# Kernel optimization log

Hardware: AMD Instinct MI355X
Metric: run time of the kernel (lower is better)

Reference implementation:

```python
import jax, jax.numpy as jnp
import numpy as np

N_INPUT = 128
N_HIDDEN = 128

def setup_inputs() -> dict:
    key = jax.random.key(0)
    k1, k2, k3, k4, k5 = jax.random.split(key, 5)
    B, T = 64, 4096
    fan1 = N_INPUT + N_HIDDEN
    s1 = 1.0 / np.sqrt(fan1)
    s2 = 1.0 / np.sqrt(N_HIDDEN)
    return {
        "input": jax.random.normal(k1, (B, T, N_INPUT), dtype=jnp.float32),
        "W1": jax.random.uniform(k2, (N_HIDDEN, fan1), jnp.float32, -s1, s1),
        "b1": jax.random.uniform(k3, (N_HIDDEN,), jnp.float32, -s1, s1),
        "W2": jax.random.uniform(k4, (N_HIDDEN, N_HIDDEN), jnp.float32, -s2, s2),
        "b2": jax.random.uniform(k5, (N_HIDDEN,), jnp.float32, -s2, s2),
    }

def reference(input, W1, b1, W2, b2):
    # input: [B, T, n_input]; carried state h: [B, n_hidden]
    B, T, _ = input.shape
    # split linear1 weight: cat order is (h, x)
    W1h = W1[:, :N_HIDDEN]   # [H, H]
    W1x = W1[:, N_HIDDEN:]   # [H, n_input]
    # precompute input projection for all timesteps: [B, T, H]
    x_proj = jnp.einsum('bti,hi->bth', input, W1x) + b1

    def step(h, xp_t):
        h_new = jax.nn.relu(h @ W1h.T + xp_t)          # [B, H]
        out = jax.nn.relu(h_new @ W2.T + b2)            # [B, H]
        return h_new, out

    h0 = jnp.zeros((B, N_HIDDEN), dtype=input.dtype)
    _, outs = jax.lax.scan(step, h0, jnp.swapaxes(x_proj, 0, 1))  # outs: [T, B, H]
    return jnp.swapaxes(outs, 0, 1)  # [B, T, H]
```

## Files before the change

kernel.cpp:

```cpp
#include <hip/hip_runtime.h>
#include <stdint.h>

#define T_LEN 4096
#define NHID  128

typedef float    f32x4 __attribute__((ext_vector_type(4)));
typedef _Float16 f16x4 __attribute__((ext_vector_type(4)));
typedef _Float16 f16x8 __attribute__((ext_vector_type(8)));
typedef __fp16   h16x2 __attribute__((ext_vector_type(2)));
typedef uint32_t u32x2 __attribute__((ext_vector_type(2)));
typedef uint32_t u32x4 __attribute__((ext_vector_type(4)));

struct P2 { h16x2 p0, p1; };
struct P4 { h16x2 p0, p1, p2, p3; };
struct U22 { u32x2 a, b; };

static __device__ __forceinline__ f16x4 cvt_f16x4(f32x4 v) {
    P2 p;
    p.p0 = __builtin_amdgcn_cvt_pkrtz(v.x, v.y);
    p.p1 = __builtin_amdgcn_cvt_pkrtz(v.z, v.w);
    return __builtin_bit_cast(f16x4, p);
}
static __device__ __forceinline__ f16x8 cvt_f16x8(f32x4 a, f32x4 b) {
    P4 p;
    p.p0 = __builtin_amdgcn_cvt_pkrtz(a.x, a.y);
    p.p1 = __builtin_amdgcn_cvt_pkrtz(a.z, a.w);
    p.p2 = __builtin_amdgcn_cvt_pkrtz(b.x, b.y);
    p.p3 = __builtin_amdgcn_cvt_pkrtz(b.z, b.w);
    return __builtin_bit_cast(f16x8, p);
}
static __device__ __forceinline__ f32x4 relu4(f32x4 v) {
    v.x = fmaxf(v.x, 0.f); v.y = fmaxf(v.y, 0.f);
    v.z = fmaxf(v.z, 0.f); v.w = fmaxf(v.w, 0.f);
    return v;
}
static __device__ __forceinline__ u32x2 relu_pk(f32x4 v) {
    P2 p;
    p.p0 = __builtin_amdgcn_cvt_pkrtz(v.x, v.y);
    p.p1 = __builtin_amdgcn_cvt_pkrtz(v.z, v.w);
    f16x4 h = __builtin_bit_cast(f16x4, p);
    const f16x4 z = {};
    h = __builtin_elementwise_max(h, z);
    return __builtin_bit_cast(u32x2, h);
}
static __device__ __forceinline__ f32x4 unpk4(u32x2 q) {
    f16x4 h = __builtin_bit_cast(f16x4, q);
    f32x4 r = { (float)h.x, (float)h.y, (float)h.z, (float)h.w };
    return r;
}
#define MFMA32(a, b, c) __builtin_amdgcn_mfma_f32_16x16x32_f16((a), (b), (c), 0, 0, 0)
#define MFMA16(a, b, c) __builtin_amdgcn_mfma_f32_16x16x16f16((a), (b), (c), 0, 0, 0)

#define LDS_BARRIER() asm volatile("s_waitcnt lgkmcnt(0)\n\ts_barrier" ::: "memory")


__global__ __launch_bounds__(64, 2)
void xproj_kernel(const float* __restrict__ input, const float* __restrict__ W1,
                  const float* __restrict__ b1, uint32_t* __restrict__ xp) {
    const int bid = blockIdx.x;
    const int g   = bid >> 8;
    const int tc  = bid & 255;
    const int l   = threadIdx.x;
    const int c   = l & 15, u = l >> 4;

    f16x8 wa[8][4];
#pragma unroll
    for (int m = 0; m < 8; ++m) {
        const float* wr = W1 + (16 * m + c) * 256 + 128 + 8 * u;
#pragma unroll
        for (int j = 0; j < 4; ++j)
            wa[m][j] = cvt_f16x8(*(const f32x4*)(wr + 32 * j),
                                 *(const f32x4*)(wr + 32 * j + 4));
    }
    f32x4 bi[8];
#pragma unroll
    for (int m = 0; m < 8; ++m) bi[m] = *(const f32x4*)(b1 + 16 * m + 4 * u);

    const int t0 = tc * 16;
    const float* ip0 = input + (size_t)(16 * g + c) * T_LEN * NHID + 8 * u;
    uint32_t* xp0 = xp + ((size_t)g * T_LEN) * 1024 + 4 * l;
#pragma unroll 1
    for (int tt = 0; tt < 16; ++tt) {
        const int t = t0 + tt;
        const float* ip = ip0 + (size_t)t * NHID;
        f16x8 xb[4];
#pragma unroll
        for (int j = 0; j < 4; ++j)
            xb[j] = cvt_f16x8(*(const f32x4*)(ip + 32 * j),
                              *(const f32x4*)(ip + 32 * j + 4));
        u32x2 pk[8];
#pragma unroll
        for (int m = 0; m < 8; ++m) {
            f32x4 a = bi[m];
#pragma unroll
            for (int j = 0; j < 4; ++j) a = MFMA32(wa[m][j], xb[j], a);
            pk[m] = __builtin_bit_cast(u32x2, cvt_f16x4(a));
        }
        uint32_t* xpt = xp0 + (size_t)t * 1024;
#pragma unroll
        for (int q = 0; q < 4; ++q) {
            U22 qq = { pk[q], pk[q + 4] };
            *(u32x4*)(xpt + q * 256) = __builtin_bit_cast(u32x4, qq);
        }
    }
}

__global__ __launch_bounds__(320, 1)
void rec_kernel(const uint32_t* __restrict__ xp, const float* __restrict__ W1,
                uint32_t* __restrict__ hg) {
    const int g  = blockIdx.x;
    const int wv = threadIdx.x >> 6;
    const int l  = threadIdx.x & 63;
    const int c  = l & 15, u = l >> 4;

    __shared__ uint32_t hbuf[2][1024];

    for (int i = threadIdx.x; i < 1024; i += 320) hbuf[0][i] = 0;
    __syncthreads();

    if (wv < 4) {
        const int w = wv;
        f16x8 waH[2][4];
#pragma unroll
        for (int e = 0; e < 2; ++e) {
            const float* wr = W1 + (16 * (w + 4 * e) + c) * 256;
#pragma unroll
            for (int kt = 0; kt < 4; ++kt)
                waH[e][kt] = cvt_f16x8(*(const f32x4*)(wr + 16 * kt + 4 * u),
                                       *(const f32x4*)(wr + 64 + 16 * kt + 4 * u));
        }

        const uint32_t* xpl = xp + ((size_t)g * T_LEN) * 1024 + w * 256 + 4 * l;

        u32x4 xr[8];
#pragma unroll
        for (int p = 0; p < 8; ++p)
            xr[p] = *(const u32x4*)(xpl + (size_t)p * 1024);

        f16x8 own;
        {
            const u32x4 z = {0, 0, 0, 0};
            own = __builtin_bit_cast(f16x8, z);
        }

#pragma unroll 1
        for (int t8 = 0; t8 < T_LEN; t8 += 8) {
#pragma unroll
            for (int p = 0; p < 8; ++p) {
                const int t   = t8 + p;
                const int par = p & 1;
                const uint32_t* rb = &hbuf[par][0];
                u32x4 r1 = *(const u32x4*)&rb[((w + 1) & 3) * 256 + 4 * l];
                u32x4 r2 = *(const u32x4*)&rb[((w + 2) & 3) * 256 + 4 * l];
                u32x4 r3 = *(const u32x4*)&rb[((w + 3) & 3) * 256 + 4 * l];
                U22 xq = __builtin_bit_cast(U22, xr[p]);
                f32x4 a0 = unpk4(xq.a);
                f32x4 a1 = unpk4(xq.b);
                a0 = MFMA32(waH[0][w], own, a0);
                a1 = MFMA32(waH[1][w], own, a1);
                f16x8 b1 = __builtin_bit_cast(f16x8, r1);
                a0 = MFMA32(waH[0][(w + 1) & 3], b1, a0);
                a1 = MFMA32(waH[1][(w + 1) & 3], b1, a1);
                f16x8 b2 = __builtin_bit_cast(f16x8, r2);
                a0 = MFMA32(waH[0][(w + 2) & 3], b2, a0);
                a1 = MFMA32(waH[1][(w + 2) & 3], b2, a1);
                f16x8 b3 = __builtin_bit_cast(f16x8, r3);
                a0 = MFMA32(waH[0][(w + 3) & 3], b3, a0);
                a1 = MFMA32(waH[1][(w + 3) & 3], b3, a1);
                u32x2 p0 = relu_pk(a0);
                u32x2 p1 = relu_pk(a1);
                U22 oq = { p0, p1 };
                own = __builtin_bit_cast(f16x8, oq);
                *(u32x4*)&hbuf[par ^ 1][w * 256 + 4 * l] =
                    __builtin_bit_cast(u32x4, oq);
                int tn = t + 8; if (tn > T_LEN - 1) tn = T_LEN - 1;
                xr[p] = *(const u32x4*)(xpl + (size_t)tn * 1024);
                LDS_BARRIER();
            }
        }
    } else {
        uint32_t* hgp = hg + ((size_t)g * T_LEN) * 1024 + 4 * l;
        u32x4 v[4][4];
#pragma unroll 1
        for (int t8 = 0; t8 < T_LEN; t8 += 8) {
#pragma unroll
            for (int p = 0; p < 8; ++p) {
                const int t   = t8 + p;
                const int par = p & 1;
                if (t > 0) {
                    const int r = p & 3;
                    const uint32_t* rb = &hbuf[par][0];
#pragma unroll
                    for (int q = 0; q < 4; ++q)
                        v[r][q] = *(const u32x4*)&rb[q * 256 + 4 * l];
                    uint32_t* hp = hgp + (size_t)(t - 1) * 1024;
#pragma unroll
                    for (int q = 0; q < 4; ++q)
                        *(u32x4*)(hp + q * 256) = v[r][q];
                }
                LDS_BARRIER();
            }
        }
        {
            const uint32_t* rb = &hbuf[0][0];
            u32x4 vf[4];
#pragma unroll
            for (int q = 0; q < 4; ++q)
                vf[q] = *(const u32x4*)&rb[q * 256 + 4 * l];
            uint32_t* hp = hgp + (size_t)(T_LEN - 1) * 1024;
#pragma unroll
            for (int q = 0; q < 4; ++q)
                *(u32x4*)(hp + q * 256) = vf[q];
        }
    }
}

__global__ __launch_bounds__(64, 2)
void out_kernel(const uint32_t* __restrict__ hg, const float* __restrict__ W2,
                const float* __restrict__ b2, float* __restrict__ out) {
    const int bid = blockIdx.x;
    const int g   = bid >> 9;
    const int tc  = bid & 511;
    const int l   = threadIdx.x;
    const int c   = l & 15, u = l >> 4;

    f16x4 wa[8][8];
#pragma unroll
    for (int m = 0; m < 8; ++m) {
        const float* wr = W2 + (16 * m + c) * 128 + 4 * u;
#pragma unroll
        for (int s = 0; s < 8; ++s)
            wa[m][s] = cvt_f16x4(*(const f32x4*)(wr + 16 * s));
    }
    f32x4 bi[8];
#pragma unroll
    for (int m = 0; m < 8; ++m) bi[m] = *(const f32x4*)(b2 + 16 * m + 4 * u);

    const int t0 = tc * 8;
    const uint32_t* hg0 = hg + ((size_t)g * T_LEN) * 1024 + 4 * l;
    float* op0 = out + (size_t)(16 * g + c) * T_LEN * NHID + 4 * u;
#pragma unroll 1
    for (int tt = 0; tt < 8; ++tt) {
        const int t = t0 + tt;
        const uint32_t* hp = hg0 + (size_t)t * 1024;
        f16x4 hb[8];
#pragma unroll
        for (int s = 0; s < 8; ++s)
            hb[s] = __builtin_bit_cast(f16x4,
                        *(const u32x2*)(hp + (s & 3) * 256 + (s >> 2) * 2));
        f32x4 acc[8];
#pragma unroll
        for (int m = 0; m < 8; ++m) {
            f32x4 a = bi[m];
#pragma unroll
            for (int s = 0; s < 8; ++s) a = MFMA16(wa[m][s], hb[s], a);
            acc[m] = relu4(a);
        }
        float* op = op0 + (size_t)t * NHID;
#pragma unroll
        for (int m = 0; m < 8; ++m) *(f32x4*)(op + 16 * m) = acc[m];
    }
}

extern "C" void kernel_launch(void* const* d_in, const int* in_sizes, int n_in,
                              void* d_out, int out_size, void* d_ws, size_t ws_size,
                              hipStream_t stream) {
    const float* input = (const float*)d_in[0];
    const float* W1    = (const float*)d_in[1];
    const float* b1    = (const float*)d_in[2];
    const float* W2    = (const float*)d_in[3];
    const float* b2    = (const float*)d_in[4];
    float*    out = (float*)d_out;
    uint32_t* xpb = (uint32_t*)d_out;
    uint32_t* hgb = (uint32_t*)d_ws;

    xproj_kernel<<<1024, 64, 0, stream>>>(input, W1, b1, xpb);
    rec_kernel  <<<4,   320, 0, stream>>>(xpb, W1, hgb);
    out_kernel  <<<2048, 64, 0, stream>>>(hgb, W2, b2, out);
}
```

Measured before the change: 1.154 ms.

## Quad-buffer hidden state, split MFMA chains, and batch writer stores every two steps

The recurrent hidden-state LDS buffer grows from two to four slots so the writer wave can fall a step behind. The writer now copies two timesteps every other step and uses a barrier without an LDS wait. In the compute waves, the accumulation is split into two independent MFMA chains summed before ReLU, which shortens the dependent chain. The next step's x-projection is unpacked early and the compute waves get raised priority. The risks are extra LDS, more register pressure, and subtle ordering hazards in the ring buffer.

After: 1.072 ms. 7.1% less time.

```diff
diff --git a/kernel.cpp b/kernel.cpp
--- a/kernel.cpp
+++ b/kernel.cpp
@@ -51,7 +51,8 @@
 #define MFMA32(a, b, c) __builtin_amdgcn_mfma_f32_16x16x32_f16((a), (b), (c), 0, 0, 0)
 #define MFMA16(a, b, c) __builtin_amdgcn_mfma_f32_16x16x16f16((a), (b), (c), 0, 0, 0)
 
-#define LDS_BARRIER() asm volatile("s_waitcnt lgkmcnt(0)\n\ts_barrier" ::: "memory")
+#define LDS_BARRIER()  asm volatile("s_waitcnt lgkmcnt(0)\n\ts_barrier" ::: "memory")
+#define BARRIER_ONLY() asm volatile("s_barrier" ::: "memory")
 
 
 __global__ __launch_bounds__(64, 2)
@@ -113,12 +114,13 @@
     const int l  = threadIdx.x & 63;
     const int c  = l & 15, u = l >> 4;
 
-    __shared__ uint32_t hbuf[2][1024];
+    __shared__ uint32_t hbuf[4][1024];
 
     for (int i = threadIdx.x; i < 1024; i += 320) hbuf[0][i] = 0;
     __syncthreads();
 
     if (wv < 4) {
+        __builtin_amdgcn_s_setprio(1);
         const int w = wv;
         f16x8 waH[2][4];
 #pragma unroll
@@ -142,36 +144,45 @@
             const u32x4 z = {0, 0, 0, 0};
             own = __builtin_bit_cast(f16x8, z);
         }
+        f32x4 xf0, xf1;
+        {
+            U22 xq = __builtin_bit_cast(U22, xr[0]);
+            xf0 = unpk4(xq.a);
+            xf1 = unpk4(xq.b);
+        }
+        const f32x4 zf = { 0.f, 0.f, 0.f, 0.f };
+        const int k1 = (w + 1) & 3, k2 = (w + 2) & 3, k3 = (w + 3) & 3;
 
 #pragma unroll 1
         for (int t8 = 0; t8 < T_LEN; t8 += 8) {
 #pragma unroll
             for (int p = 0; p < 8; ++p) {
-                const int t   = t8 + p;
-                const int par = p & 1;
-                const uint32_t* rb = &hbuf[par][0];
-                u32x4 r1 = *(const u32x4*)&rb[((w + 1) & 3) * 256 + 4 * l];
-                u32x4 r2 = *(const u32x4*)&rb[((w + 2) & 3) * 256 + 4 * l];
-                u32x4 r3 = *(const u32x4*)&rb[((w + 3) & 3) * 256 + 4 * l];
-                U22 xq = __builtin_bit_cast(U22, xr[p]);
-                f32x4 a0 = unpk4(xq.a);
-                f32x4 a1 = unpk4(xq.b);
-                a0 = MFMA32(waH[0][w], own, a0);
-                a1 = MFMA32(waH[1][w], own, a1);
+                const int t = t8 + p;
+                const uint32_t* rb = &hbuf[p & 3][0];
+                u32x4 r1 = *(const u32x4*)&rb[k1 * 256 + 4 * l];
+                u32x4 r2 = *(const u32x4*)&rb[k2 * 256 + 4 * l];
+                u32x4 r3 = *(const u32x4*)&rb[k3 * 256 + 4 * l];
+                f32x4 a0a = MFMA32(waH[0][w], own, xf0);
+                f32x4 a1a = MFMA32(waH[1][w], own, xf1);
+                {
+                    U22 xq = __builtin_bit_cast(U22, xr[(p + 1) & 7]);
+                    xf0 = unpk4(xq.a);
+                    xf1 = unpk4(xq.b);
+                }
                 f16x8 b1 = __builtin_bit_cast(f16x8, r1);
-                a0 = MFMA32(waH[0][(w + 1) & 3], b1, a0);
-                a1 = MFMA32(waH[1][(w + 1) & 3], b1, a1);
+                f32x4 a0b = MFMA32(waH[0][k1], b1, zf);
+                f32x4 a1b = MFMA32(waH[1][k1], b1, zf);
                 f16x8 b2 = __builtin_bit_cast(f16x8, r2);
-                a0 = MFMA32(waH[0][(w + 2) & 3], b2, a0);
-                a1 = MFMA32(waH[1][(w + 2) & 3], b2, a1);
+                a0a = MFMA32(waH[0][k2], b2, a0a);
+                a1a = MFMA32(waH[1][k2], b2, a1a);
                 f16x8 b3 = __builtin_bit_cast(f16x8, r3);
-                a0 = MFMA32(waH[0][(w + 3) & 3], b3, a0);
-                a1 = MFMA32(waH[1][(w + 3) & 3], b3, a1);
-                u32x2 p0 = relu_pk(a0);
-                u32x2 p1 = relu_pk(a1);
+                a0b = MFMA32(waH[0][k3], b3, a0b);
+                a1b = MFMA32(waH[1][k3], b3, a1b);
+                u32x2 p0 = relu_pk(a0a + a0b);
+                u32x2 p1 = relu_pk(a1a + a1b);
                 U22 oq = { p0, p1 };
                 own = __builtin_bit_cast(f16x8, oq);
-                *(u32x4*)&hbuf[par ^ 1][w * 256 + 4 * l] =
+                *(u32x4*)&hbuf[(p + 1) & 3][w * 256 + 4 * l] =
                     __builtin_bit_cast(u32x4, oq);
                 int tn = t + 8; if (tn > T_LEN - 1) tn = T_LEN - 1;
                 xr[p] = *(const u32x4*)(xpl + (size_t)tn * 1024);
@@ -180,25 +191,34 @@
         }
     } else {
         uint32_t* hgp = hg + ((size_t)g * T_LEN) * 1024 + 4 * l;
-        u32x4 v[4][4];
+        u32x4 v[2][8];
 #pragma unroll 1
         for (int t8 = 0; t8 < T_LEN; t8 += 8) {
 #pragma unroll
             for (int p = 0; p < 8; ++p) {
-                const int t   = t8 + p;
-                const int par = p & 1;
-                if (t > 0) {
-                    const int r = p & 3;
-                    const uint32_t* rb = &hbuf[par][0];
+                const int t = t8 + p;
+                if (p & 1) {
+                    const int r = (p >> 1) & 1;
+                    const uint32_t* rbA = &hbuf[p & 3][0];
+                    const uint32_t* rbB = &hbuf[(p - 1) & 3][0];
 #pragma unroll
                     for (int q = 0; q < 4; ++q)
-                        v[r][q] = *(const u32x4*)&rb[q * 256 + 4 * l];
-                    uint32_t* hp = hgp + (size_t)(t - 1) * 1024;
+                        v[r][q] = *(const u32x4*)&rbA[q * 256 + 4 * l];
 #pragma unroll
                     for (int q = 0; q < 4; ++q)
-                        *(u32x4*)(hp + q * 256) = v[r][q];
+                        v[r][4 + q] = *(const u32x4*)&rbB[q * 256 + 4 * l];
+                    uint32_t* hpA = hgp + (size_t)(t - 1) * 1024;
+#pragma unroll
+                    for (int q = 0; q < 4; ++q)
+                        *(u32x4*)(hpA + q * 256) = v[r][q];
+                    if (t > 1) {
+                        uint32_t* hpB = hgp + (size_t)(t - 2) * 1024;
+#pragma unroll
+                        for (int q = 0; q < 4; ++q)
+                            *(u32x4*)(hpB + q * 256) = v[r][4 + q];
+                    }
                 }
-                LDS_BARRIER();
+                BARRIER_ONLY();
             }
         }
         {
```
